# Performance work log

Measured on AMD Instinct MI355X. Metric: run time of the kernel, lower is better.

## Reference

```python
import jax, jax.numpy as jnp
import numpy as np

B, S, HIDDEN = 2, 2048, 2048
NUM_HEADS = 16
HEAD_DIM = 128
ROPE_BASE = 10000.0


def _rope_cos_sin(positions):
    # positions: [B, S] int -> cos/sin [B, 1, S, HEAD_DIM]
    inv_freq = 1.0 / (ROPE_BASE ** (jnp.arange(0, HEAD_DIM, 2, dtype=jnp.float32) / HEAD_DIM))
    freqs = positions.astype(jnp.float32)[..., None] * inv_freq  # [B, S, D/2]
    emb = jnp.concatenate([freqs, freqs], axis=-1)  # [B, S, D]
    return jnp.cos(emb)[:, None, :, :], jnp.sin(emb)[:, None, :, :]


def _rotate_half(x, cos, sin):
    half = x.shape[-1] // 2
    x1, x2 = x[..., :half], x[..., half:]
    return jnp.concatenate([-x2, x1], axis=-1) * sin + x * cos


def setup_inputs() -> dict:
    key = jax.random.key(0)
    ks = jax.random.split(key, 6)
    hidden_states = jax.random.normal(ks[0], (B, S, HIDDEN), dtype=jnp.float32)
    positions = jnp.arange(B * S, dtype=jnp.int64 if jax.config.x64_enabled else jnp.int32).reshape(B, S)
    scale = 0.02
    Wq = jax.random.normal(ks[1], (HIDDEN, NUM_HEADS * HEAD_DIM), dtype=jnp.float32) * scale
    Wk = jax.random.normal(ks[2], (HIDDEN, NUM_HEADS * HEAD_DIM), dtype=jnp.float32) * scale
    Wv = jax.random.normal(ks[3], (HIDDEN, NUM_HEADS * HEAD_DIM), dtype=jnp.float32) * scale
    Wo = jax.random.normal(ks[4], (NUM_HEADS * HEAD_DIM, HIDDEN), dtype=jnp.float32) * scale
    bq = jnp.zeros((NUM_HEADS * HEAD_DIM,), dtype=jnp.float32)
    bk = jnp.zeros((NUM_HEADS * HEAD_DIM,), dtype=jnp.float32)
    bv = jnp.zeros((NUM_HEADS * HEAD_DIM,), dtype=jnp.float32)
    return {"positions": positions, "hidden_states": hidden_states,
            "Wq": Wq, "bq": bq, "Wk": Wk, "bk": bk, "Wv": Wv, "bv": bv, "Wo": Wo}


def reference(positions, hidden_states, Wq, bq, Wk, bk, Wv, bv, Wo):
    b, s, _ = hidden_states.shape
    # projections
    q = hidden_states @ Wq + bq  # [B, S, H*D]
    k = hidden_states @ Wk + bk
    v = hidden_states @ Wv + bv
    # -> [B, H, S, D]
    q = q.reshape(b, s, NUM_HEADS, HEAD_DIM).transpose(0, 2, 1, 3)
    k = k.reshape(b, s, NUM_HEADS, HEAD_DIM).transpose(0, 2, 1, 3)
    v = v.reshape(b, s, NUM_HEADS, HEAD_DIM).transpose(0, 2, 1, 3)
    # RoPE
    cos, sin = _rope_cos_sin(positions)
    q = _rotate_half(q, cos, sin)
    k = _rotate_half(k, cos, sin)
    # scaled dot-product attention (no mask)
    scaling = HEAD_DIM ** -0.5
    scores = jnp.einsum('bhqd,bhkd->bhqk', q, k) * scaling
    attn = jax.nn.softmax(scores, axis=-1)
    out = jnp.einsum('bhqk,bhkd->bhqd', attn, v)
    out = out.transpose(0, 2, 1, 3).reshape(b, s, NUM_HEADS * HEAD_DIM)
    return out @ Wo
```

## Files before the change

kernel.cpp:

```cpp
#include <hip/hip_runtime.h>
#include <cstdint>
#include <cstddef>

typedef unsigned short u16;
typedef __attribute__((ext_vector_type(8))) unsigned short u16x8;
typedef __attribute__((ext_vector_type(8))) short bf16x8;
typedef __attribute__((ext_vector_type(4))) float f32x4;

#define MFMA_BF16(a, b, c) __builtin_amdgcn_mfma_f32_16x16x32_bf16((a), (b), (c), 0, 0, 0)

__device__ __forceinline__ u16 f2bf(float f) {
  union { float f; uint32_t u; } v; v.f = f;
  uint32_t r = v.u + 0x7fffu + ((v.u >> 16) & 1u);
  return (u16)(r >> 16);
}
__device__ __forceinline__ float bf2f(u16 u) {
  union { uint32_t u; float f; } v; v.u = ((uint32_t)u) << 16;
  return v.f;
}
__device__ __forceinline__ void gl2lds16(const void* g, void* l) {
  __builtin_amdgcn_global_load_lds((__attribute__((address_space(1))) const void*)g,
                                   (__attribute__((address_space(3))) void*)l, 16, 0, 0);
}


__global__ __launch_bounds__(256) void cvt_kernel(const float* __restrict__ in,
                                                  u16* __restrict__ out) {
  int idx = blockIdx.x * 256 + threadIdx.x;
  float4 a = ((const float4*)in)[(size_t)idx * 2];
  float4 b = ((const float4*)in)[(size_t)idx * 2 + 1];
  u16x8 o;
  o[0] = f2bf(a.x); o[1] = f2bf(a.y); o[2] = f2bf(a.z); o[3] = f2bf(a.w);
  o[4] = f2bf(b.x); o[5] = f2bf(b.y); o[6] = f2bf(b.z); o[7] = f2bf(b.w);
  *(u16x8*)(out + (size_t)idx * 8) = o;
}

__global__ __launch_bounds__(256) void trans_kernel(const float* __restrict__ in,
                                                    u16* __restrict__ out) {
  __shared__ float tile[64][65];
  int t = threadIdx.x;
  int r0 = blockIdx.y * 64, c0 = blockIdx.x * 64;
#pragma unroll
  for (int i = 0; i < 16; ++i) {
    int idx = i * 256 + t; int r = idx >> 6, c = idx & 63;
    tile[r][c] = in[(size_t)(r0 + r) * 2048 + c0 + c];
  }
  __syncthreads();
#pragma unroll
  for (int i = 0; i < 16; ++i) {
    int idx = i * 256 + t; int r = idx >> 6, c = idx & 63;
    out[(size_t)(c0 + r) * 2048 + r0 + c] = f2bf(tile[c][r]);
  }
}

__global__ __launch_bounds__(256) void rope_table_kernel(const int* __restrict__ pos,
                                                         float* __restrict__ cosT,
                                                         float* __restrict__ sinT) {
  int idx = blockIdx.x * 256 + threadIdx.x;
  int i = idx & 63, t = idx >> 6;
  double ang = (double)pos[t] * exp(-(double)i * (9.210340371976184 / 64.0));
  double s, c;
  sincos(ang, &s, &c);
  cosT[idx] = (float)c;
  sinT[idx] = (float)s;
}

__global__ __launch_bounds__(256) void rope_kernel(u16* __restrict__ Q,
                                                   u16* __restrict__ Kk,
                                                   const float* __restrict__ cosT,
                                                   const float* __restrict__ sinT) {
  int idx = blockIdx.x * 256 + threadIdx.x;
  int d = idx & 63, h = (idx >> 6) & 15, tok = idx >> 10;
  int b = tok >> 11, s = tok & 2047;
  size_t base = ((size_t)((b * 16 + h) * 2048 + s)) * 128;
  float c = cosT[(tok << 6) + d], sn = sinT[(tok << 6) + d];
  const float sc = 0.08838834764831845f;
  float q1 = bf2f(Q[base + d]), q2 = bf2f(Q[base + d + 64]);
  Q[base + d]      = f2bf((q1 * c - q2 * sn) * sc);
  Q[base + d + 64] = f2bf((q2 * c + q1 * sn) * sc);
  float k1 = bf2f(Kk[base + d]), k2 = bf2f(Kk[base + d + 64]);
  Kk[base + d]      = f2bf(k1 * c - k2 * sn);
  Kk[base + d + 64] = f2bf(k2 * c + k1 * sn);
}

__global__ __launch_bounds__(256) void vtrans_kernel(const u16* __restrict__ V,
                                                     u16* __restrict__ Vt) {
  __shared__ u16 tile[128][72];
  int t = threadIdx.x;
  int bh = blockIdx.x >> 5, st = blockIdx.x & 31;
  const u16* src = V + ((size_t)bh * 2048 + st * 64) * 128;
#pragma unroll
  for (int i = 0; i < 4; ++i) {
    int idx = i * 256 + t;
    int s = idx >> 4;
    int d0 = (idx & 15) << 3;
    u16x8 v = *(const u16x8*)(src + (size_t)s * 128 + d0);
#pragma unroll
    for (int j = 0; j < 8; ++j) tile[d0 + j][s] = v[j];
  }
  __syncthreads();
  u16* dst = Vt + (size_t)bh * 128 * 2048 + st * 64;
#pragma unroll
  for (int i = 0; i < 4; ++i) {
    int idx = i * 256 + t;
    int d = idx >> 3;
    int s0 = (idx & 7) << 3;
    u16x8 o;
#pragma unroll
    for (int j = 0; j < 8; ++j) o[j] = tile[d][s0 + j];
    *(u16x8*)(dst + (size_t)d * 2048 + s0) = o;
  }
}


__global__ __launch_bounds__(256) void gemm1_kernel(
    const u16* __restrict__ A,
    const u16* __restrict__ Bt,
    const float* __restrict__ bq, const float* __restrict__ bk, const float* __restrict__ bv,
    u16* __restrict__ Qo, u16* __restrict__ Ko, u16* __restrict__ Vo) {
  __shared__ u16 sA[128 * 32], sB[128 * 32];
  const int K = 2048;
  int t = threadIdx.x, lane = t & 63, wid = t >> 6;
  int bm = blockIdx.x & 31, bn = blockIdx.x >> 5;
  int m0 = bm << 7, n0 = bn << 7;
  int wr = wid >> 1, wc = wid & 1;
  int fr = lane & 15, fq = lane >> 4;

  const f32x4 vzero = {0.f, 0.f, 0.f, 0.f};
  f32x4 acc[4][4];
#pragma unroll
  for (int m = 0; m < 4; ++m)
#pragma unroll
    for (int n = 0; n < 4; ++n) acc[m][n] = vzero;

  int arow = t >> 2, acol = (t & 3) << 3;
  const u16* ga0 = A + (size_t)(m0 + arow) * K + acol;
  const u16* ga1 = ga0 + (size_t)64 * K;
  const u16* gb0 = Bt + (size_t)(n0 + arow) * K + acol;
  const u16* gb1 = gb0 + (size_t)64 * K;
  u16* lA0 = sA + t * 8; u16* lA1 = sA + 2048 + t * 8;
  u16* lB0 = sB + t * 8; u16* lB1 = sB + 2048 + t * 8;

  for (int k0 = 0; k0 < K; k0 += 32) {
    gl2lds16(ga0 + k0, lA0);
    gl2lds16(ga1 + k0, lA1);
    gl2lds16(gb0 + k0, lB0);
    gl2lds16(gb1 + k0, lB1);
    __syncthreads();
    bf16x8 af[4], bfv[4];
#pragma unroll
    for (int m = 0; m < 4; ++m)
      af[m] = *(const bf16x8*)(sA + ((wr * 64 + m * 16 + fr) * 32 + fq * 8));
#pragma unroll
    for (int n = 0; n < 4; ++n)
      bfv[n] = *(const bf16x8*)(sB + ((wc * 64 + n * 16 + fr) * 32 + fq * 8));
#pragma unroll
    for (int m = 0; m < 4; ++m)
#pragma unroll
      for (int n = 0; n < 4; ++n)
        acc[m][n] = MFMA_BF16(af[m], bfv[n], acc[m][n]);
    __syncthreads();
  }
#pragma unroll
  for (int n = 0; n < 4; ++n) {
    int col = n0 + wc * 64 + n * 16 + fr;
    int which = col >> 11;
    int cin = col & 2047;
    const float* bp = (which == 0) ? bq : (which == 1) ? bk : bv;
    u16* dst = (which == 0) ? Qo : (which == 1) ? Ko : Vo;
    float bias = bp[cin];
    int h = cin >> 7, d = cin & 127;
#pragma unroll
    for (int m = 0; m < 4; ++m) {
      int row = m0 + wr * 64 + m * 16 + fq * 4;
#pragma unroll
      for (int r = 0; r < 4; ++r) {
        int tok = row + r;
        int b = tok >> 11, s = tok & 2047;
        dst[((size_t)((b * 16 + h) * 2048 + s) << 7) + d] = f2bf(acc[m][n][r] + bias);
      }
    }
  }
}

__global__ __launch_bounds__(256) void gemm2_kernel(
    const u16* __restrict__ A,
    const u16* __restrict__ Bt,
    float* __restrict__ C) {
  __shared__ u16 sA[128 * 32], sB[128 * 32];
  const int K = 2048;
  int t = threadIdx.x, lane = t & 63, wid = t >> 6;
  int bm = blockIdx.x & 31, bn = blockIdx.x >> 5;
  int m0 = bm << 7, n0 = bn << 7;
  int wr = wid >> 1, wc = wid & 1;
  int fr = lane & 15, fq = lane >> 4;

  const f32x4 vzero = {0.f, 0.f, 0.f, 0.f};
  f32x4 acc[4][4];
#pragma unroll
  for (int m = 0; m < 4; ++m)
#pragma unroll
    for (int n = 0; n < 4; ++n) acc[m][n] = vzero;

  int arow = t >> 2, acol = (t & 3) << 3;
  const u16* ga0 = A + (size_t)(m0 + arow) * K + acol;
  const u16* ga1 = ga0 + (size_t)64 * K;
  const u16* gb0 = Bt + (size_t)(n0 + arow) * K + acol;
  const u16* gb1 = gb0 + (size_t)64 * K;
  u16* lA0 = sA + t * 8; u16* lA1 = sA + 2048 + t * 8;
  u16* lB0 = sB + t * 8; u16* lB1 = sB + 2048 + t * 8;

  for (int k0 = 0; k0 < K; k0 += 32) {
    gl2lds16(ga0 + k0, lA0);
    gl2lds16(ga1 + k0, lA1);
    gl2lds16(gb0 + k0, lB0);
    gl2lds16(gb1 + k0, lB1);
    __syncthreads();
    bf16x8 af[4], bfv[4];
#pragma unroll
    for (int m = 0; m < 4; ++m)
      af[m] = *(const bf16x8*)(sA + ((wr * 64 + m * 16 + fr) * 32 + fq * 8));
#pragma unroll
    for (int n = 0; n < 4; ++n)
      bfv[n] = *(const bf16x8*)(sB + ((wc * 64 + n * 16 + fr) * 32 + fq * 8));
#pragma unroll
    for (int m = 0; m < 4; ++m)
#pragma unroll
      for (int n = 0; n < 4; ++n)
        acc[m][n] = MFMA_BF16(af[m], bfv[n], acc[m][n]);
    __syncthreads();
  }
#pragma unroll
  for (int n = 0; n < 4; ++n) {
    int col = n0 + wc * 64 + n * 16 + fr;
#pragma unroll
    for (int m = 0; m < 4; ++m) {
      int row = m0 + wr * 64 + m * 16 + fq * 4;
#pragma unroll
      for (int r = 0; r < 4; ++r)
        C[(size_t)(row + r) * 2048 + col] = acc[m][n][r];
    }
  }
}

__global__ __launch_bounds__(512) void attn_kernel(
    const u16* __restrict__ Q_,
    const u16* __restrict__ K_,
    const u16* __restrict__ Vt_,
    u16* __restrict__ AO) {
  __shared__ u16 sK[2][64 * 128];
  __shared__ u16 sV[2][128 * 64];
  __shared__ u16 sP[8][32 * 64];
  int t = threadIdx.x, lane = t & 63, wid = t >> 6;
  int fr = lane & 15, fq = lane >> 4;
  int qt = blockIdx.x & 7, bh = blockIdx.x >> 3;
  int q0 = qt << 8;
  const u16* Qb = Q_ + (size_t)bh * 2048 * 128;
  const char* Kc = (const char*)(K_ + (size_t)bh * 2048 * 128);
  const char* Vc = (const char*)(Vt_ + (size_t)bh * 128 * 2048);

  bf16x8 qf[2][4];
#pragma unroll
  for (int m = 0; m < 2; ++m) {
    const u16* qp = Qb + (size_t)(q0 + wid * 32 + m * 16 + fr) * 128 + fq * 8;
#pragma unroll
    for (int kk = 0; kk < 4; ++kk) qf[m][kk] = *(const bf16x8*)(qp + kk * 32);
  }

  int kgoff[2], kldst[2], vgoff[2], vldst[2];
#pragma unroll
  for (int i = 0; i < 2; ++i) {
    int kr = i * 32 + (t >> 4);
    kgoff[i] = kr * 256 + (((t & 15) << 4) ^ ((kr & 7) << 4));
    kldst[i] = i * 8192 + t * 16;
    int vr = i * 64 + (t >> 3);
    vgoff[i] = vr * 4096 + (((t & 7) << 4) ^ ((vr & 7) << 4));
    vldst[i] = i * 8192 + t * 16;
  }

#define STAGE(tt, bb)                                                          \
  {                                                                            \
    size_t ko = (size_t)(tt) * 16384;                                          \
    size_t vo = (size_t)(tt) * 128;                                            \
    _Pragma("unroll")                                                          \
    for (int i = 0; i < 2; ++i)                                                \
      gl2lds16(Kc + ko + kgoff[i], (char*)sK[bb] + kldst[i]);                  \
    _Pragma("unroll")                                                          \
    for (int i = 0; i < 2; ++i)                                                \
      gl2lds16(Vc + vo + vgoff[i], (char*)sV[bb] + vldst[i]);                  \
  }

  float mrun[2][4], lrun[2][4];
#pragma unroll
  for (int m = 0; m < 2; ++m)
#pragma unroll
    for (int r = 0; r < 4; ++r) { mrun[m][r] = -1e30f; lrun[m][r] = 0.f; }
  const f32x4 vzero = {0.f, 0.f, 0.f, 0.f};
  f32x4 oacc[2][8];
#pragma unroll
  for (int m = 0; m < 2; ++m)
#pragma unroll
    for (int fd = 0; fd < 8; ++fd) oacc[m][fd] = vzero;

  char* sPw = (char*)sP[wid];

  STAGE(0, 0);
  __syncthreads();

  for (int tile = 0; tile < 32; ++tile) {
    int cur = tile & 1;
    if (tile < 31) STAGE(tile + 1, cur ^ 1);
    const char* Kb_ = (const char*)sK[cur];
    const char* Vb_ = (const char*)sV[cur];

    f32x4 sacc[2][4];
#pragma unroll
    for (int m = 0; m < 2; ++m)
#pragma unroll
      for (int n = 0; n < 4; ++n) sacc[m][n] = vzero;
    __builtin_amdgcn_s_setprio(1);
#pragma unroll
    for (int n = 0; n < 4; ++n) {
      int krow = n * 16 + fr;
      int swz = (krow & 7) << 4;
      const char* kbase = Kb_ + krow * 256;
#pragma unroll
      for (int kk = 0; kk < 4; ++kk) {
        bf16x8 kf = *(const bf16x8*)(kbase + ((kk * 64 + fq * 16) ^ swz));
        sacc[0][n] = MFMA_BF16(qf[0][kk], kf, sacc[0][n]);
        sacc[1][n] = MFMA_BF16(qf[1][kk], kf, sacc[1][n]);
      }
    }
    __builtin_amdgcn_s_setprio(0);

    float pmax[2][4];
#pragma unroll
    for (int m = 0; m < 2; ++m)
#pragma unroll
      for (int r = 0; r < 4; ++r) {
        float v = fmaxf(fmaxf(sacc[m][0][r], sacc[m][1][r]),
                        fmaxf(sacc[m][2][r], sacc[m][3][r]));
        v = fmaxf(v, __shfl_xor(v, 1));
        v = fmaxf(v, __shfl_xor(v, 2));
        v = fmaxf(v, __shfl_xor(v, 4));
        v = fmaxf(v, __shfl_xor(v, 8));
        pmax[m][r] = v;
      }
    int ok = 1;
#pragma unroll
    for (int m = 0; m < 2; ++m)
#pragma unroll
      for (int r = 0; r < 4; ++r)
        ok &= (pmax[m][r] <= mrun[m][r] + 8.f) ? 1 : 0;
    if (!__all(ok)) {
#pragma unroll
      for (int m = 0; m < 2; ++m)
#pragma unroll
        for (int r = 0; r < 4; ++r) {
          float mn = fmaxf(mrun[m][r], pmax[m][r]);
          float scl = __expf(mrun[m][r] - mn);
          mrun[m][r] = mn;
          lrun[m][r] *= scl;
#pragma unroll
          for (int fd = 0; fd < 8; ++fd) oacc[m][fd][r] *= scl;
        }
    }
    float rs[2][4] = {{0.f, 0.f, 0.f, 0.f}, {0.f, 0.f, 0.f, 0.f}};
#pragma unroll
    for (int m = 0; m < 2; ++m)
#pragma unroll
      for (int n = 0; n < 4; ++n)
#pragma unroll
        for (int r = 0; r < 4; ++r) {
          float p = __expf(sacc[m][n][r] - mrun[m][r]);
          rs[m][r] += p;
          int q = m * 16 + fq * 4 + r;
          *(u16*)(sPw + q * 128 + ((((n * 16 + fr) << 1)) ^ ((q & 7) << 4))) = f2bf(p);
        }
#pragma unroll
    for (int m = 0; m < 2; ++m)
#pragma unroll
      for (int r = 0; r < 4; ++r) {
        float s = rs[m][r];
        s += __shfl_xor(s, 1);
        s += __shfl_xor(s, 2);
        s += __shfl_xor(s, 4);
        s += __shfl_xor(s, 8);
        lrun[m][r] += s;
      }

    bf16x8 pf[2][2];
#pragma unroll
    for (int m = 0; m < 2; ++m)
#pragma unroll
      for (int kk = 0; kk < 2; ++kk)
        pf[m][kk] = *(const bf16x8*)(sPw + (m * 16 + fr) * 128 +
                                     ((kk * 64 + fq * 16) ^ ((fr & 7) << 4)));
    __builtin_amdgcn_s_setprio(1);
#pragma unroll
    for (int fd = 0; fd < 8; ++fd) {
      int vrow = fd * 16 + fr;
      int vswz = (vrow & 7) << 4;
      const char* vbase = Vb_ + vrow * 128;
#pragma unroll
      for (int kk = 0; kk < 2; ++kk) {
        bf16x8 vf = *(const bf16x8*)(vbase + ((kk * 64 + fq * 16) ^ vswz));
        oacc[0][fd] = MFMA_BF16(pf[0][kk], vf, oacc[0][fd]);
        oacc[1][fd] = MFMA_BF16(pf[1][kk], vf, oacc[1][fd]);
      }
    }
    __builtin_amdgcn_s_setprio(0);
    __syncthreads();
  }
#undef STAGE

  int h = bh & 15, b = bh >> 4;
#pragma unroll
  for (int m = 0; m < 2; ++m)
#pragma unroll
    for (int r = 0; r < 4; ++r) {
      float inv = 1.f / lrun[m][r];
      int tok = b * 2048 + q0 + wid * 32 + m * 16 + fq * 4 + r;
#pragma unroll
      for (int fd = 0; fd < 8; ++fd) {
        int col = h * 128 + fd * 16 + fr;
        AO[(size_t)tok * 2048 + col] = f2bf(oacc[m][fd][r] * inv);
      }
    }
}


extern "C" void kernel_launch(void* const* d_in, const int* in_sizes, int n_in,
                              void* d_out, int out_size, void* d_ws, size_t ws_size,
                              hipStream_t stream) {
  (void)in_sizes; (void)n_in; (void)out_size; (void)ws_size;
  const int*   positions = (const int*)d_in[0];
  const float* hidden    = (const float*)d_in[1];
  const float* Wq = (const float*)d_in[2];
  const float* bq = (const float*)d_in[3];
  const float* Wk = (const float*)d_in[4];
  const float* bk = (const float*)d_in[5];
  const float* Wv = (const float*)d_in[6];
  const float* bv = (const float*)d_in[7];
  const float* Wo = (const float*)d_in[8];
  float* out = (float*)d_out;

  char* ws = (char*)d_ws;
  u16*   Xb   = (u16*)(ws);
  u16*   Wt   = (u16*)(ws + 16777216);
  u16*   Wot  = (u16*)(ws + 41943040);
  u16*   Qb   = (u16*)(ws + 50331648);
  u16*   Kb   = (u16*)(ws + 67108864);
  u16*   Vb   = (u16*)(ws + 83886080);
  u16*   Vtb  = (u16*)(ws + 100663296);
  u16*   AO   = (u16*)(ws + 117440512);
  float* cosT = (float*)(ws + 134217728);
  float* sinT = (float*)(ws + 135266304);

  cvt_kernel<<<4096, 256, 0, stream>>>(hidden, Xb);
  trans_kernel<<<dim3(32, 32), 256, 0, stream>>>(Wq, Wt);
  trans_kernel<<<dim3(32, 32), 256, 0, stream>>>(Wk, Wt + (size_t)2048 * 2048);
  trans_kernel<<<dim3(32, 32), 256, 0, stream>>>(Wv, Wt + (size_t)2 * 2048 * 2048);
  trans_kernel<<<dim3(32, 32), 256, 0, stream>>>(Wo, Wot);
  rope_table_kernel<<<1024, 256, 0, stream>>>(positions, cosT, sinT);
  gemm1_kernel<<<1536, 256, 0, stream>>>(Xb, Wt, bq, bk, bv, Qb, Kb, Vb);
  rope_kernel<<<16384, 256, 0, stream>>>(Qb, Kb, cosT, sinT);
  vtrans_kernel<<<1024, 256, 0, stream>>>(Vb, Vtb);
  attn_kernel<<<256, 512, 0, stream>>>(Qb, Kb, Vtb, AO);
  gemm2_kernel<<<512, 256, 0, stream>>>(AO, Wot, out);
}
```

Measured before the change: 473.7 us.

## Vectorize transpose and RoPE kernels, merge weight transposes, remap GEMM block order

```diff
diff --git a/kernel.cpp b/kernel.cpp
--- a/kernel.cpp
+++ b/kernel.cpp
@@ -35,21 +35,32 @@
   *(u16x8*)(out + (size_t)idx * 8) = o;
 }
 
-__global__ __launch_bounds__(256) void trans_kernel(const float* __restrict__ in,
-                                                    u16* __restrict__ out) {
+__global__ __launch_bounds__(256) void trans_kernel(
+    const float* __restrict__ W0, const float* __restrict__ W1,
+    const float* __restrict__ W2, const float* __restrict__ W3,
+    u16* __restrict__ out0, u16* __restrict__ out3) {
   __shared__ float tile[64][65];
+  int z = blockIdx.z;
+  const float* in = (z == 0) ? W0 : (z == 1) ? W1 : (z == 2) ? W2 : W3;
+  u16* out = (z == 3) ? out3 : out0 + (size_t)z * 2048 * 2048;
   int t = threadIdx.x;
   int r0 = blockIdx.y * 64, c0 = blockIdx.x * 64;
 #pragma unroll
-  for (int i = 0; i < 16; ++i) {
-    int idx = i * 256 + t; int r = idx >> 6, c = idx & 63;
-    tile[r][c] = in[(size_t)(r0 + r) * 2048 + c0 + c];
+  for (int i = 0; i < 4; ++i) {
+    int idx = i * 256 + t;
+    int r = idx >> 4, c4 = (idx & 15) << 2;
+    float4 v = *(const float4*)(in + (size_t)(r0 + r) * 2048 + c0 + c4);
+    tile[r][c4] = v.x; tile[r][c4 + 1] = v.y; tile[r][c4 + 2] = v.z; tile[r][c4 + 3] = v.w;
   }
   __syncthreads();
 #pragma unroll
-  for (int i = 0; i < 16; ++i) {
-    int idx = i * 256 + t; int r = idx >> 6, c = idx & 63;
-    out[(size_t)(c0 + r) * 2048 + r0 + c] = f2bf(tile[c][r]);
+  for (int i = 0; i < 2; ++i) {
+    int idx = i * 256 + t;
+    int orr = idx >> 3, oc8 = (idx & 7) << 3;
+    u16x8 o;
+#pragma unroll
+    for (int j = 0; j < 8; ++j) o[j] = f2bf(tile[oc8 + j][orr]);
+    *(u16x8*)(out + (size_t)(c0 + orr) * 2048 + r0 + oc8) = o;
   }
 }
 
@@ -70,17 +81,36 @@
                                                    const float* __restrict__ cosT,
                                                    const float* __restrict__ sinT) {
   int idx = blockIdx.x * 256 + threadIdx.x;
-  int d = idx & 63, h = (idx >> 6) & 15, tok = idx >> 10;
+  int d8 = (idx & 7) << 3;
+  int h = (idx >> 3) & 15;
+  int tok = idx >> 7;
   int b = tok >> 11, s = tok & 2047;
   size_t base = ((size_t)((b * 16 + h) * 2048 + s)) * 128;
-  float c = cosT[(tok << 6) + d], sn = sinT[(tok << 6) + d];
+  const float* cp = cosT + (tok << 6) + d8;
+  const float* sp = sinT + (tok << 6) + d8;
+  float4 c0 = *(const float4*)cp, c1 = *(const float4*)(cp + 4);
+  float4 s0 = *(const float4*)sp, s1 = *(const float4*)(sp + 4);
+  float cc[8] = {c0.x, c0.y, c0.z, c0.w, c1.x, c1.y, c1.z, c1.w};
+  float ss[8] = {s0.x, s0.y, s0.z, s0.w, s1.x, s1.y, s1.z, s1.w};
   const float sc = 0.08838834764831845f;
-  float q1 = bf2f(Q[base + d]), q2 = bf2f(Q[base + d + 64]);
-  Q[base + d]      = f2bf((q1 * c - q2 * sn) * sc);
-  Q[base + d + 64] = f2bf((q2 * c + q1 * sn) * sc);
-  float k1 = bf2f(Kk[base + d]), k2 = bf2f(Kk[base + d + 64]);
-  Kk[base + d]      = f2bf(k1 * c - k2 * sn);
-  Kk[base + d + 64] = f2bf(k2 * c + k1 * sn);
+  u16x8 q1 = *(const u16x8*)(Q + base + d8);
+  u16x8 q2 = *(const u16x8*)(Q + base + 64 + d8);
+  u16x8 k1 = *(const u16x8*)(Kk + base + d8);
+  u16x8 k2 = *(const u16x8*)(Kk + base + 64 + d8);
+  u16x8 o1, o2, p1, p2;
+#pragma unroll
+  for (int j = 0; j < 8; ++j) {
+    float a = bf2f(q1[j]), bb = bf2f(q2[j]);
+    o1[j] = f2bf((a * cc[j] - bb * ss[j]) * sc);
+    o2[j] = f2bf((bb * cc[j] + a * ss[j]) * sc);
+    float x = bf2f(k1[j]), y = bf2f(k2[j]);
+    p1[j] = f2bf(x * cc[j] - y * ss[j]);
+    p2[j] = f2bf(y * cc[j] + x * ss[j]);
+  }
+  *(u16x8*)(Q + base + d8) = o1;
+  *(u16x8*)(Q + base + 64 + d8) = o2;
+  *(u16x8*)(Kk + base + d8) = p1;
+  *(u16x8*)(Kk + base + 64 + d8) = p2;
 }
 
 __global__ __launch_bounds__(256) void vtrans_kernel(const u16* __restrict__ V,
@@ -121,7 +151,8 @@
   __shared__ u16 sA[128 * 32], sB[128 * 32];
   const int K = 2048;
   int t = threadIdx.x, lane = t & 63, wid = t >> 6;
-  int bm = blockIdx.x & 31, bn = blockIdx.x >> 5;
+  int bid = (blockIdx.x & 7) * 192 + (blockIdx.x >> 3);
+  int bm = bid / 48, bn = bid % 48;
   int m0 = bm << 7, n0 = bn << 7;
   int wr = wid >> 1, wc = wid & 1;
   int fr = lane & 15, fq = lane >> 4;
@@ -190,7 +221,8 @@
   __shared__ u16 sA[128 * 32], sB[128 * 32];
   const int K = 2048;
   int t = threadIdx.x, lane = t & 63, wid = t >> 6;
-  int bm = blockIdx.x & 31, bn = blockIdx.x >> 5;
+  int bid = (blockIdx.x & 7) * 64 + (blockIdx.x >> 3);
+  int bm = bid >> 4, bn = bid & 15;
   int m0 = bm << 7, n0 = bn << 7;
   int wr = wid >> 1, wc = wid & 1;
   int fr = lane & 15, fq = lane >> 4;
@@ -458,13 +490,10 @@
   float* sinT = (float*)(ws + 135266304);
 
   cvt_kernel<<<4096, 256, 0, stream>>>(hidden, Xb);
-  trans_kernel<<<dim3(32, 32), 256, 0, stream>>>(Wq, Wt);
-  trans_kernel<<<dim3(32, 32), 256, 0, stream>>>(Wk, Wt + (size_t)2048 * 2048);
-  trans_kernel<<<dim3(32, 32), 256, 0, stream>>>(Wv, Wt + (size_t)2 * 2048 * 2048);
-  trans_kernel<<<dim3(32, 32), 256, 0, stream>>>(Wo, Wot);
+  trans_kernel<<<dim3(32, 32, 4), 256, 0, stream>>>(Wq, Wk, Wv, Wo, Wt, Wot);
   rope_table_kernel<<<1024, 256, 0, stream>>>(positions, cosT, sinT);
   gemm1_kernel<<<1536, 256, 0, stream>>>(Xb, Wt, bq, bk, bv, Qb, Kb, Vb);
-  rope_kernel<<<16384, 256, 0, stream>>>(Qb, Kb, cosT, sinT);
+  rope_kernel<<<2048, 256, 0, stream>>>(Qb, Kb, cosT, sinT);
   vtrans_kernel<<<1024, 256, 0, stream>>>(Vb, Vtb);
   attn_kernel<<<256, 512, 0, stream>>>(Qb, Kb, Vtb, AO);
   gemm2_kernel<<<512, 256, 0, stream>>>(AO, Wot, out);
```

Result: slower. 498.2 us (+5.2%).
